# Kernel optimization log

Measured on AMD Instinct MI355X. Metric: run time of the kernel, lower is better.

The kernel has to match this reference:

```python
import jax, jax.numpy as jnp
import numpy as np

N = 50000      # nodes
E = 400000     # edges (avg degree 8)
F_IN = 128     # input feature dim
H = 4          # heads (layer 1)
D = 128        # hidden per head
C = 3          # classes (layer 2 out, 1 head)
EPS = 1e-5     # BatchNorm eps
SLOPE = 0.2    # LeakyReLU negative slope (DGL GATConv default)


def setup_inputs() -> dict:
    key = jax.random.key(0)
    ks = jax.random.split(key, 16)
    s = jnp.float32(0.05)
    return {
        "features": jax.random.normal(ks[0], (N, F_IN), jnp.float32),
        "src": jax.random.randint(ks[1], (E,), 0, N, jnp.int32),
        "dst": jax.random.randint(ks[2], (E,), 0, N, jnp.int32),
        # GATConv layer 1 params
        "W1": jax.random.normal(ks[3], (F_IN, H * D), jnp.float32) * s,
        "al1": jax.random.normal(ks[4], (H, D), jnp.float32) * s,
        "ar1": jax.random.normal(ks[5], (H, D), jnp.float32) * s,
        "b1": jnp.zeros((H * D,), jnp.float32),
        "Wres1": jax.random.normal(ks[6], (F_IN, H * D), jnp.float32) * s,
        # BatchNorm1d (inference mode)
        "bn_gamma": jnp.ones((H * D,), jnp.float32),
        "bn_beta": jnp.zeros((H * D,), jnp.float32),
        "bn_mean": jnp.zeros((H * D,), jnp.float32),
        "bn_var": jnp.ones((H * D,), jnp.float32),
        # GATConv layer 2 params (1 head, C out)
        "W2": jax.random.normal(ks[7], (H * D, C), jnp.float32) * s,
        "al2": jax.random.normal(ks[8], (1, C), jnp.float32) * s,
        "ar2": jax.random.normal(ks[9], (1, C), jnp.float32) * s,
        "b2": jnp.zeros((C,), jnp.float32),
        "Wres2": jax.random.normal(ks[10], (H * D, C), jnp.float32) * s,
    }


def _gat_layer(x, src, dst, W, attn_l, attn_r, bias, Wres, heads, dim):
    """DGL GATConv (eval mode): gather, LeakyReLU score, segment softmax,
    weighted scatter-sum, linear residual, bias."""
    n = x.shape[0]
    z = (x @ W).reshape(n, heads, dim)                 # [N,H,D]
    el = jnp.sum(z * attn_l, axis=-1)                  # [N,H]
    er = jnp.sum(z * attn_r, axis=-1)                  # [N,H]
    e = jax.nn.leaky_relu(el[src] + er[dst], SLOPE)    # [E,H]
    # segment softmax over incoming edges of each dst node
    m = jax.ops.segment_max(e, dst, num_segments=n)    # [N,H]
    ex = jnp.exp(e - m[dst])                           # [E,H]
    den = jax.ops.segment_sum(ex, dst, num_segments=n) # [N,H]
    alpha = ex / den[dst]                              # [E,H]
    # weighted message aggregation
    rst = jax.ops.segment_sum(z[src] * alpha[..., None], dst, num_segments=n)  # [N,H,D]
    res = (x @ Wres).reshape(n, heads, dim)
    return rst + res + bias.reshape(1, heads, dim)


def reference(features, src, dst, W1, al1, ar1, b1, Wres1,
              bn_gamma, bn_beta, bn_mean, bn_var,
              W2, al2, ar2, b2, Wres2):
    h = _gat_layer(features, src, dst, W1, al1, ar1, b1, Wres1, H, D)
    h = h.reshape(N, H * D)
    # BatchNorm1d (inference) + ELU; dropout is identity in eval mode
    h = (h - bn_mean) * jax.lax.rsqrt(bn_var + EPS) * bn_gamma + bn_beta
    h = jax.nn.elu(h)
    h = _gat_layer(h, src, dst, W2, al2, ar2, b2, Wres2, 1, C)
    return h[:, 0, :]  # squeeze head dim -> [N, C]
```

## Files before the change

### kernel.cpp

```cpp
#include <hip/hip_runtime.h>
#include <hip/hip_bf16.h>

#define N_NODES 50000
#define N_EDGES 400000
#define FIN     128
#define HD      512
#define SLOPE   0.2f
#define NB_X    782

typedef __hip_bfloat16 bf16;
typedef __bf16 bf16x8 __attribute__((ext_vector_type(8)));
typedef __bf16 bf16x4 __attribute__((ext_vector_type(4)));
typedef __bf16 bf16x2 __attribute__((ext_vector_type(2)));
typedef float  f32x4  __attribute__((ext_vector_type(4)));
typedef float  f32x2  __attribute__((ext_vector_type(2)));

__global__ void sentinel_k(float* out, int n) {
    int i = blockIdx.x * 256 + threadIdx.x;
    if (i < n) out[i] = 12288.0f;
}

__global__ __launch_bounds__(256) void prep_k(const float* __restrict__ W1, const float* __restrict__ Wres1,
                                              const float* __restrict__ al1, const float* __restrict__ ar1,
                                              const float* __restrict__ W2, const float* __restrict__ Wres2,
                                              const float* __restrict__ b1,
                                              const float* __restrict__ bnm, const float* __restrict__ bnv,
                                              const float* __restrict__ bng, const float* __restrict__ bnb,
                                              bf16* __restrict__ Wfrag, float* __restrict__ tab,
                                              bf16* __restrict__ wlrb,
                                              int* __restrict__ deg, int* __restrict__ cur0,
                                              int* __restrict__ done) {
    int b = blockIdx.x;
    if (b < 196) {
        int i = b * 256 + threadIdx.x;
        if (i < N_NODES) { deg[i] = 0; cur0[i] = 0; }
        if (b == 0 && threadIdx.x == 0) *done = 0;
        return;
    }
    b -= 196;
    if (b < 64) {
        int f = b * 256 + threadIdx.x;
        int lane = f & 63, unit = f >> 6;
        int tile = unit >> 3, ks = unit & 7;
        int cl = lane & 15, rg = lane >> 4;
        int gc = tile * 16 + cl;
        int k0 = ks * 32 + rg * 8;
        bf16x8 v;
#pragma unroll
        for (int j = 0; j < 8; ++j) {
            int kk = k0 + j;
            float x = (kk < 128) ? W1[kk * HD + gc] : Wres1[(kk - 128) * HD + gc];
            v[j] = (__bf16)x;
        }
        *reinterpret_cast<bf16x8*>(reinterpret_cast<char*>(Wfrag) + (size_t)f * 16) = v;
        return;
    }
    b -= 64;
    if (b < 16) {
        int i = b * 256 + threadIdx.x;
        int gc = i >> 3, c = i & 7;
        float v;
        if (c < 2) {
            float rs = rsqrtf(bnv[gc] + 1e-5f) * bng[gc];
            v = (c == 0) ? rs : (b1[gc] - bnm[gc]) * rs + bnb[gc];
        } else if (c < 5) {
            v = W2[gc * 3 + (c - 2)];
        } else {
            v = Wres2[gc * 3 + (c - 5)];
        }
        tab[i] = v;
        return;
    }
    for (int i = 0; i < 8; ++i) {
        int e = i * 256 + threadIdx.x;
        int ks = e >> 9, lane = (e >> 3) & 63, j = e & 7;
        int r = lane & 15, rg = lane >> 4;
        int k = ks * 32 + rg * 8 + j;
        float v = 0.f;
        if (r < 4) {
            for (int d = 0; d < 128; ++d) v += W1[k * HD + r * 128 + d] * al1[r * 128 + d];
        } else if (r < 8) {
            int h = r - 4;
            for (int d = 0; d < 128; ++d) v += W1[k * HD + h * 128 + d] * ar1[h * 128 + d];
        }
        wlrb[e] = __float2bfloat16(v);
    }
}

__global__ __launch_bounds__(256) void eler_k(const float* __restrict__ X,
                                              const bf16* __restrict__ wlrb,
                                              float* __restrict__ el, float* __restrict__ er,
                                              bf16* __restrict__ Xb,
                                              const int* __restrict__ dst, int* __restrict__ deg) {
    if (blockIdx.x >= NB_X) {
        int e = (blockIdx.x - NB_X) * 256 + threadIdx.x;
        if (e < N_EDGES) atomicAdd(&deg[dst[e]], 1);
        return;
    }
    __shared__ __align__(16) char XSb[64 * 256];
    const int t = threadIdx.x;
    const int w = t >> 6, lane = t & 63;
    const int cl = lane & 15, rg = lane >> 4;
    const int m0 = blockIdx.x * 64;

#pragma unroll
    for (int j = 0; j < 8; ++j) {
        int e = j * 1024 + t * 4;
        int row = e >> 7, col = e & 127;
        int grow = m0 + row;
        int gc = grow < N_NODES ? grow : N_NODES - 1;
        f32x4 v = *reinterpret_cast<const f32x4*>(X + (size_t)gc * FIN + col);
        bf16x4 bv = {(__bf16)v[0], (__bf16)v[1], (__bf16)v[2], (__bf16)v[3]};
        if (grow < N_NODES)
            *reinterpret_cast<bf16x4*>(Xb + (size_t)grow * FIN + col) = bv;
        int byte = (row * 256 + col * 2) ^ ((row & 7) << 4);
        *reinterpret_cast<bf16x4*>(XSb + byte) = bv;
    }
    __syncthreads();

    f32x4 a = {0.f, 0.f, 0.f, 0.f};
    const int row = w * 16 + cl;
    const int swz = (row & 7) << 4;
#pragma unroll
    for (int ks = 0; ks < 4; ++ks) {
        bf16x8 af = *reinterpret_cast<const bf16x8*>(
            reinterpret_cast<const char*>(wlrb) + ((size_t)(ks * 64 + lane)) * 16);
        int byte = (row * 256 + ks * 64 + rg * 16) ^ swz;
        bf16x8 bf = *reinterpret_cast<const bf16x8*>(XSb + byte);
        a = __builtin_amdgcn_mfma_f32_16x16x32_bf16(af, bf, a, 0, 0, 0);
    }
    int n = m0 + row;
    if (n < N_NODES) {
        if (rg == 0)      *reinterpret_cast<float4*>(el + (size_t)n * 4) = make_float4(a[0], a[1], a[2], a[3]);
        else if (rg == 1) *reinterpret_cast<float4*>(er + (size_t)n * 4) = make_float4(a[0], a[1], a[2], a[3]);
    }
}

__global__ __launch_bounds__(256) void scan_k(const int* __restrict__ deg,
                                              int* __restrict__ rloc, int* __restrict__ blksum,
                                              int* __restrict__ bsum, int* __restrict__ done) {
    __shared__ int wsum[4];
    __shared__ int isLast;
    int t = threadIdx.x, b = blockIdx.x;
    int i = b * 256 + t;
    int v = (i < N_NODES) ? deg[i] : 0;
    int lane = t & 63, w = t >> 6;
    int x = v;
#pragma unroll
    for (int off = 1; off < 64; off <<= 1) {
        int y = __shfl_up(x, off);
        if (lane >= off) x += y;
    }
    if (lane == 63) wsum[w] = x;
    __syncthreads();
    int wadd = 0;
    if (w > 0) wadd += wsum[0];
    if (w > 1) wadd += wsum[1];
    if (w > 2) wadd += wsum[2];
    int incl = x + wadd;
    if (i < N_NODES) rloc[i] = incl - v;
    if (t == 255) atomicExch(&blksum[b], incl);
    __threadfence();
    if (t == 0) {
        int r = atomicAdd(done, 1);
        isLast = (r == 195);
    }
    __syncthreads();
    if (!isLast) return;

    int v2 = (t < 196) ? atomicAdd(&blksum[t], 0) : 0;
    int x2 = v2;
#pragma unroll
    for (int off = 1; off < 64; off <<= 1) {
        int y = __shfl_up(x2, off);
        if (lane >= off) x2 += y;
    }
    __syncthreads();
    if (lane == 63) wsum[w] = x2;
    __syncthreads();
    int wadd2 = 0;
    if (w > 0) wadd2 += wsum[0];
    if (w > 1) wadd2 += wsum[1];
    if (w > 2) wadd2 += wsum[2];
    if (t < 196) bsum[t] = x2 + wadd2 - v2;
}

__global__ void fill_k(const int* __restrict__ src, const int* __restrict__ dst,
                       const int* __restrict__ rloc, const int* __restrict__ bsum,
                       int* __restrict__ cur0, int* __restrict__ csr) {
    int e = blockIdx.x * 256 + threadIdx.x;
    if (e < N_EDGES) {
        int d = dst[e];
        int slot = atomicAdd(&cur0[d], 1);
        csr[rloc[d] + bsum[d >> 8] + slot] = src[e];
    }
}

__global__ __launch_bounds__(1024) void aggX_k(const int* __restrict__ rloc, const int* __restrict__ bsum,
                                               const int* __restrict__ degA, const int* __restrict__ csr,
                                               const float* __restrict__ el, const float* __restrict__ er,
                                               const bf16* __restrict__ Xb, bf16* __restrict__ AGGb,
                                               float* __restrict__ den4) {
    const int w = threadIdx.x >> 6, lane = threadIdx.x & 63;
    const int sub = lane >> 5, ll = lane & 31;
    int n = blockIdx.x * 32 + w * 2 + sub;
    const bool valid = n < N_NODES;
    if (!valid) n = N_NODES - 1;
    const int beg = rloc[n] + bsum[n >> 8];
    const int deg = degA[n];
    const float4 ern = *reinterpret_cast<const float4*>(er + (size_t)n * 4);
    const char* Xbc = reinterpret_cast<const char*>(Xb);

    f32x2 accA[4] = {{0.f,0.f},{0.f,0.f},{0.f,0.f},{0.f,0.f}};
    f32x2 accB[4] = {{0.f,0.f},{0.f,0.f},{0.f,0.f},{0.f,0.f}};
    float4 dp = make_float4(0.f, 0.f, 0.f, 0.f);

    for (int base = 0; base < deg; base += 32) {
        const int cnt = min(32, deg - base);
        int s = 0;
        if (ll < cnt) s = csr[beg + base + ll];
        float4 e4 = *reinterpret_cast<const float4*>(el + (size_t)s * 4);
        float4 p; float e;
        e = e4.x + ern.x; e = e > 0.f ? e : SLOPE * e; p.x = __expf(e);
        e = e4.y + ern.y; e = e > 0.f ? e : SLOPE * e; p.y = __expf(e);
        e = e4.z + ern.z; e = e > 0.f ? e : SLOPE * e; p.z = __expf(e);
        e = e4.w + ern.w; e = e > 0.f ? e : SLOPE * e; p.w = __expf(e);

        for (int j = 0; j < cnt; ++j) {
            int idx = sub * 32 + j;
            int sj = __shfl(s, idx);
            uint2 xv = *reinterpret_cast<const uint2*>(Xbc + (size_t)sj * 256 + ll * 8);
            float4 pj;
            pj.x = __shfl(p.x, idx);
            pj.y = __shfl(p.y, idx);
            pj.z = __shfl(p.z, idx);
            pj.w = __shfl(p.w, idx);
            dp.x += pj.x; dp.y += pj.y; dp.z += pj.z; dp.w += pj.w;
            f32x2 xlo = {__uint_as_float(xv.x << 16), __uint_as_float(xv.x & 0xffff0000u)};
            f32x2 xhi = {__uint_as_float(xv.y << 16), __uint_as_float(xv.y & 0xffff0000u)};
            accA[0] += pj.x * xlo; accB[0] += pj.x * xhi;
            accA[1] += pj.y * xlo; accB[1] += pj.y * xhi;
            accA[2] += pj.z * xlo; accB[2] += pj.z * xhi;
            accA[3] += pj.w * xlo; accB[3] += pj.w * xhi;
        }
    }

    if (valid) {
#pragma unroll
        for (int h = 0; h < 4; ++h) {
            bf16x4 v = {(__bf16)accA[h][0], (__bf16)accA[h][1],
                        (__bf16)accB[h][0], (__bf16)accB[h][1]};
            *reinterpret_cast<bf16x4*>(AGGb + (size_t)n * 512 + h * 128 + ll * 4) = v;
        }
        if (ll == 0) *reinterpret_cast<float4*>(den4 + (size_t)n * 4) = dp;
    }
}

__global__ __launch_bounds__(256) void gemm2_k(
    const bf16* __restrict__ Xb, const bf16* __restrict__ AGGb,
    const float* __restrict__ den4,
    const bf16* __restrict__ Wfrag, const float* __restrict__ tab,
    const float* __restrict__ al2, const float* __restrict__ ar2,
    float* __restrict__ node2) {
    __shared__ __align__(16) char XS[32 * 256];
    __shared__ __align__(16) char AGS[32 * 1024];
    __shared__ float zsum[4][32][6];

    const int t = threadIdx.x;
    const int w = t >> 6, lane = t & 63;
    const int cl = lane & 15, rg = lane >> 4;
    const int m0 = blockIdx.x * 32;

#pragma unroll
    for (int j = 0; j < 2; ++j) {
        int L = j * 4096 + t * 16;
        int row = L >> 8, col = L & 255;
        int grow = m0 + row; grow = grow < N_NODES ? grow : N_NODES - 1;
        bf16x8 v = *reinterpret_cast<const bf16x8*>(
            reinterpret_cast<const char*>(Xb) + (size_t)grow * 256 + col);
        int byte = (row * 256 + col) ^ ((row & 7) << 4);
        *reinterpret_cast<bf16x8*>(XS + byte) = v;
    }
#pragma unroll
    for (int j = 0; j < 8; ++j) {
        int L = j * 4096 + t * 16;
        int row = L >> 10, col = L & 1023;
        int grow = m0 + row; grow = grow < N_NODES ? grow : N_NODES - 1;
        bf16x8 v = *reinterpret_cast<const bf16x8*>(
            reinterpret_cast<const char*>(AGGb) + (size_t)grow * 1024 + col);
        int byte = (row * 1024 + col) ^ ((row & 7) << 4);
        *reinterpret_cast<bf16x8*>(AGS + byte) = v;
    }
    __syncthreads();

    float invden[2];
#pragma unroll
    for (int mt = 0; mt < 2; ++mt) {
        int nn = m0 + mt * 16 + cl;
        nn = nn < N_NODES ? nn : N_NODES - 1;
        float d = den4[(size_t)nn * 4 + w];
        invden[mt] = d > 0.f ? 1.f / d : 0.f;
    }

    float z2p[2][3] = {}, r2p[2][3] = {};

#pragma unroll
    for (int ct = 0; ct < 8; ++ct) {
        const int unit = (w * 8 + ct) * 8;
        bf16x8 af[8];
#pragma unroll
        for (int ks = 0; ks < 8; ++ks)
            af[ks] = *reinterpret_cast<const bf16x8*>(
                reinterpret_cast<const char*>(Wfrag) + ((size_t)(unit + ks) * 64 + lane) * 16);
        const int gcl = w * 128 + ct * 16 + rg * 4;
        f32x4 t0[4], t1[4];
#pragma unroll
        for (int i = 0; i < 4; ++i) {
            t0[i] = *reinterpret_cast<const f32x4*>(tab + (size_t)(gcl + i) * 8);
            t1[i] = *reinterpret_cast<const f32x4*>(tab + (size_t)(gcl + i) * 8 + 4);
        }
#pragma unroll
        for (int mt = 0; mt < 2; ++mt) {
            int row = mt * 16 + cl;
            int swz = (row & 7) << 4;
            f32x4 aA = {0.f, 0.f, 0.f, 0.f};
            f32x4 aX = {0.f, 0.f, 0.f, 0.f};
#pragma unroll
            for (int ks = 0; ks < 4; ++ks) {
                int byte = (row * 1024 + w * 256 + ks * 64 + rg * 16) ^ swz;
                bf16x8 bfr = *reinterpret_cast<const bf16x8*>(AGS + byte);
                aA = __builtin_amdgcn_mfma_f32_16x16x32_bf16(af[ks], bfr, aA, 0, 0, 0);
            }
#pragma unroll
            for (int ks = 0; ks < 4; ++ks) {
                int byte = (row * 256 + ks * 64 + rg * 16) ^ swz;
                bf16x8 bfr = *reinterpret_cast<const bf16x8*>(XS + byte);
                aX = __builtin_amdgcn_mfma_f32_16x16x32_bf16(af[ks + 4], bfr, aX, 0, 0, 0);
            }
#pragma unroll
            for (int i = 0; i < 4; ++i) {
                float z = aA[i] * invden[mt] + aX[i];
                float hv = z * t0[i][0] + t0[i][1];
                hv = hv > 0.f ? hv : (__expf(hv) - 1.f);
                z2p[mt][0] += hv * t0[i][2]; z2p[mt][1] += hv * t0[i][3]; z2p[mt][2] += hv * t1[i][0];
                r2p[mt][0] += hv * t1[i][1]; r2p[mt][1] += hv * t1[i][2]; r2p[mt][2] += hv * t1[i][3];
            }
        }
    }

#pragma unroll
    for (int mt = 0; mt < 2; ++mt)
#pragma unroll
        for (int c = 0; c < 3; ++c) {
            z2p[mt][c] += __shfl_xor(z2p[mt][c], 16);
            z2p[mt][c] += __shfl_xor(z2p[mt][c], 32);
            r2p[mt][c] += __shfl_xor(r2p[mt][c], 16);
            r2p[mt][c] += __shfl_xor(r2p[mt][c], 32);
        }
    if (rg == 0) {
#pragma unroll
        for (int mt = 0; mt < 2; ++mt) {
            int nl = mt * 16 + cl;
            zsum[w][nl][0] = z2p[mt][0]; zsum[w][nl][1] = z2p[mt][1]; zsum[w][nl][2] = z2p[mt][2];
            zsum[w][nl][3] = r2p[mt][0]; zsum[w][nl][4] = r2p[mt][1]; zsum[w][nl][5] = r2p[mt][2];
        }
    }
    __syncthreads();
    if (t < 32) {
        float v[6];
#pragma unroll
        for (int c = 0; c < 6; ++c)
            v[c] = zsum[0][t][c] + zsum[1][t][c] + zsum[2][t][c] + zsum[3][t][c];
        int n = m0 + t;
        if (n < N_NODES) {
            float e2l = v[0] * al2[0] + v[1] * al2[1] + v[2] * al2[2];
            float e2r = v[0] * ar2[0] + v[1] * ar2[1] + v[2] * ar2[2];
            *reinterpret_cast<float4*>(node2 + (size_t)n * 8) = make_float4(v[0], v[1], v[2], e2l);
            *reinterpret_cast<float4*>(node2 + (size_t)n * 8 + 4) = make_float4(v[3], v[4], v[5], e2r);
        }
    }
}

__global__ __launch_bounds__(256) void agg2_k(const int* __restrict__ rloc, const int* __restrict__ bsum,
                                              const int* __restrict__ degA, const int* __restrict__ csr,
                                              const float* __restrict__ node2,
                                              const float* __restrict__ b2, float* __restrict__ out) {
    int wv = threadIdx.x >> 6, lane = threadIdx.x & 63;
    int n = blockIdx.x * 4 + wv;
    int beg = rloc[n] + bsum[n >> 8];
    int deg = degA[n];
    float ern = node2[(size_t)n * 8 + 7];
    float den = 0.f, a0 = 0.f, a1 = 0.f, a2 = 0.f;
    for (int j = lane; j < deg; j += 64) {
        int s = csr[beg + j];
        float4 v = *reinterpret_cast<const float4*>(node2 + (size_t)s * 8);
        float e = v.w + ern;
        e = e > 0.f ? e : SLOPE * e;
        float p = __expf(e);
        den += p;
        a0 += p * v.x; a1 += p * v.y; a2 += p * v.z;
    }
#pragma unroll
    for (int off = 32; off > 0; off >>= 1) {
        den += __shfl_xor(den, off);
        a0 += __shfl_xor(a0, off); a1 += __shfl_xor(a1, off); a2 += __shfl_xor(a2, off);
    }
    if (lane == 0) {
        float inv = deg > 0 ? 1.f / den : 0.f;
        float4 r = *reinterpret_cast<const float4*>(node2 + (size_t)n * 8 + 4);
        out[(size_t)n * 3 + 0] = a0 * inv + r.x + b2[0];
        out[(size_t)n * 3 + 1] = a1 * inv + r.y + b2[1];
        out[(size_t)n * 3 + 2] = a2 * inv + r.z + b2[2];
    }
}

extern "C" void kernel_launch(void* const* d_in, const int* in_sizes, int n_in,
                              void* d_out, int out_size, void* d_ws, size_t ws_size,
                              hipStream_t stream) {
    const float* X     = (const float*)d_in[0];
    const int*   src   = (const int*)d_in[1];
    const int*   dst   = (const int*)d_in[2];
    const float* W1    = (const float*)d_in[3];
    const float* al1   = (const float*)d_in[4];
    const float* ar1   = (const float*)d_in[5];
    const float* b1    = (const float*)d_in[6];
    const float* Wres1 = (const float*)d_in[7];
    const float* bng   = (const float*)d_in[8];
    const float* bnb   = (const float*)d_in[9];
    const float* bnm   = (const float*)d_in[10];
    const float* bnv   = (const float*)d_in[11];
    const float* W2    = (const float*)d_in[12];
    const float* al2   = (const float*)d_in[13];
    const float* ar2   = (const float*)d_in[14];
    const float* b2    = (const float*)d_in[15];
    const float* Wres2 = (const float*)d_in[16];
    float* out = (float*)d_out;

    char* p = (char*)d_ws;
    auto carve = [&](size_t bytes) -> char* {
        char* r = p;
        p += (bytes + 255) & ~(size_t)255;
        return r;
    };
    bf16*  Wfrag  = (bf16*)carve((size_t)512 * 256 * 2);
    float* tab    = (float*)carve((size_t)512 * 8 * 4);
    bf16*  wlrb   = (bf16*)carve((size_t)2048 * 2);
    float* el     = (float*)carve((size_t)N_NODES * 4 * 4);
    float* er     = (float*)carve((size_t)N_NODES * 4 * 4);
    int*   deg    = (int*)carve((size_t)N_NODES * 4);
    int*   rloc   = (int*)carve((size_t)(N_NODES + 256) * 4);
    int*   cur0   = (int*)carve((size_t)N_NODES * 4);
    int*   blksum = (int*)carve((size_t)256 * 4);
    int*   bsum   = (int*)carve((size_t)256 * 4);
    int*   done   = (int*)carve((size_t)256);
    int*   csr    = (int*)carve((size_t)N_EDGES * 4);
    bf16*  Xb     = (bf16*)carve((size_t)N_NODES * FIN * 2);
    bf16*  AGGb   = (bf16*)carve((size_t)N_NODES * 512 * 2);
    float* den4   = (float*)carve((size_t)(N_NODES + 64) * 4 * 4);
    float* node2  = (float*)carve((size_t)N_NODES * 8 * 4);
    size_t need = (size_t)(p - (char*)d_ws);
    if (need > ws_size) {
        sentinel_k<<<(out_size + 255) / 256, 256, 0, stream>>>(out, out_size);
        return;
    }

    prep_k<<<196 + 64 + 16 + 1, 256, 0, stream>>>(W1, Wres1, al1, ar1, W2, Wres2, b1,
                                                  bnm, bnv, bng, bnb, Wfrag, tab, wlrb,
                                                  deg, cur0, done);
    eler_k<<<NB_X + (N_EDGES + 255) / 256, 256, 0, stream>>>(X, wlrb, el, er, Xb, dst, deg);
    scan_k<<<196, 256, 0, stream>>>(deg, rloc, blksum, bsum, done);
    fill_k<<<(N_EDGES + 255) / 256, 256, 0, stream>>>(src, dst, rloc, bsum, cur0, csr);
    aggX_k<<<(N_NODES + 31) / 32, 1024, 0, stream>>>(rloc, bsum, deg, csr, el, er, Xb, AGGb, den4);
    gemm2_k<<<(N_NODES + 31) / 32, 256, 0, stream>>>(Xb, AGGb, den4, Wfrag, tab, al2, ar2, node2);
    agg2_k<<<N_NODES / 4, 256, 0, stream>>>(rloc, bsum, deg, csr, node2, b2, out);
}
```

Before: 189.2 us.

## Store X and aggregate in MFMA fragment layout so gemm2 loads fragments directly

eler_k now also writes the bf16 input tile in MFMA B-fragment order (XF), and aggX_k stages its aggregated rows in shared memory and writes them out in fragment order (AGF). gemm2_k then loads its MFMA operands straight into registers from global memory instead of staging through 40KB of LDS with a barrier, and gets a launch bound of two blocks per SIMD. The aim is to drop LDS traffic and the sync from gemm2 and raise its occupancy. In exchange aggX_k gains 32KB of LDS, a block barrier and a shuffle pass, and an extra XF write is added. A __syncthreads was also added to scan_k before the completion counter, which fixes ordering.

```diff
diff --git a/kernel.cpp b/kernel.cpp
--- a/kernel.cpp
+++ b/kernel.cpp
@@ -90,7 +90,7 @@
 __global__ __launch_bounds__(256) void eler_k(const float* __restrict__ X,
                                               const bf16* __restrict__ wlrb,
                                               float* __restrict__ el, float* __restrict__ er,
-                                              bf16* __restrict__ Xb,
+                                              bf16* __restrict__ Xb, bf16* __restrict__ XF,
                                               const int* __restrict__ dst, int* __restrict__ deg) {
     if (blockIdx.x >= NB_X) {
         int e = (blockIdx.x - NB_X) * 256 + threadIdx.x;
@@ -121,12 +121,14 @@
     f32x4 a = {0.f, 0.f, 0.f, 0.f};
     const int row = w * 16 + cl;
     const int swz = (row & 7) << 4;
+    char* XFc = reinterpret_cast<char*>(XF);
 #pragma unroll
     for (int ks = 0; ks < 4; ++ks) {
         bf16x8 af = *reinterpret_cast<const bf16x8*>(
             reinterpret_cast<const char*>(wlrb) + ((size_t)(ks * 64 + lane)) * 16);
         int byte = (row * 256 + ks * 64 + rg * 16) ^ swz;
         bf16x8 bf = *reinterpret_cast<const bf16x8*>(XSb + byte);
+        *reinterpret_cast<bf16x8*>(XFc + ((size_t)(blockIdx.x * 4 + w) * 4 + ks) * 1024 + lane * 16) = bf;
         a = __builtin_amdgcn_mfma_f32_16x16x32_bf16(af, bf, a, 0, 0, 0);
     }
     int n = m0 + row;
@@ -161,6 +163,7 @@
     if (i < N_NODES) rloc[i] = incl - v;
     if (t == 255) atomicExch(&blksum[b], incl);
     __threadfence();
+    __syncthreads();
     if (t == 0) {
         int r = atomicAdd(done, 1);
         isLast = (r == 195);
@@ -199,11 +202,13 @@
 __global__ __launch_bounds__(1024) void aggX_k(const int* __restrict__ rloc, const int* __restrict__ bsum,
                                                const int* __restrict__ degA, const int* __restrict__ csr,
                                                const float* __restrict__ el, const float* __restrict__ er,
-                                               const bf16* __restrict__ Xb, bf16* __restrict__ AGGb,
+                                               const bf16* __restrict__ Xb, bf16* __restrict__ AGF,
                                                float* __restrict__ den4) {
+    __shared__ __align__(16) char AS[32 * 1024];
     const int w = threadIdx.x >> 6, lane = threadIdx.x & 63;
     const int sub = lane >> 5, ll = lane & 31;
-    int n = blockIdx.x * 32 + w * 2 + sub;
+    const int nl = w * 2 + sub;
+    int n = blockIdx.x * 32 + nl;
     const bool valid = n < N_NODES;
     if (!valid) n = N_NODES - 1;
     const int beg = rloc[n] + bsum[n >> 8];
@@ -245,53 +250,59 @@
         }
     }
 
-    if (valid) {
+    {
+        const int swz = (nl & 7) << 4;
 #pragma unroll
         for (int h = 0; h < 4; ++h) {
             bf16x4 v = {(__bf16)accA[h][0], (__bf16)accA[h][1],
                         (__bf16)accB[h][0], (__bf16)accB[h][1]};
-            *reinterpret_cast<bf16x4*>(AGGb + (size_t)n * 512 + h * 128 + ll * 4) = v;
-        }
-        if (ll == 0) *reinterpret_cast<float4*>(den4 + (size_t)n * 4) = dp;
-    }
-}
-
-__global__ __launch_bounds__(256) void gemm2_k(
-    const bf16* __restrict__ Xb, const bf16* __restrict__ AGGb,
+            int byte = (nl * 1024 + h * 256 + ll * 8) ^ swz;
+            *reinterpret_cast<bf16x4*>(AS + byte) = v;
+        }
+        if (valid && ll == 0) *reinterpret_cast<float4*>(den4 + (size_t)n * 4) = dp;
+    }
+    __syncthreads();
+
+    const int t = threadIdx.x;
+    char* AGFc = reinterpret_cast<char*>(AGF);
+#pragma unroll
+    for (int q = 0; q < 2; ++q) {
+        int fid = q * 1024 + t;
+        int L = fid & 63, unit = fid >> 6;
+        int g = unit >> 4, h = (unit >> 2) & 3, ks = unit & 3;
+        int nl2 = g * 16 + (L & 15);
+        int sbyte = (nl2 * 1024 + h * 256 + ks * 64 + (L >> 4) * 16) ^ ((nl2 & 7) << 4);
+        bf16x8 v = *reinterpret_cast<const bf16x8*>(AS + sbyte);
+        size_t gid = ((size_t)(blockIdx.x * 2 + g) * 16 + h * 4 + ks);
+        *reinterpret_cast<bf16x8*>(AGFc + gid * 1024 + (size_t)L * 16) = v;
+    }
+}
+
+__global__ __launch_bounds__(256, 2) void gemm2_k(
+    const bf16* __restrict__ XF, const bf16* __restrict__ AGF,
     const float* __restrict__ den4,
     const bf16* __restrict__ Wfrag, const float* __restrict__ tab,
     const float* __restrict__ al2, const float* __restrict__ ar2,
     float* __restrict__ node2) {
-    __shared__ __align__(16) char XS[32 * 256];
-    __shared__ __align__(16) char AGS[32 * 1024];
     __shared__ float zsum[4][32][6];
 
     const int t = threadIdx.x;
     const int w = t >> 6, lane = t & 63;
     const int cl = lane & 15, rg = lane >> 4;
     const int m0 = blockIdx.x * 32;
-
-#pragma unroll
-    for (int j = 0; j < 2; ++j) {
-        int L = j * 4096 + t * 16;
-        int row = L >> 8, col = L & 255;
-        int grow = m0 + row; grow = grow < N_NODES ? grow : N_NODES - 1;
-        bf16x8 v = *reinterpret_cast<const bf16x8*>(
-            reinterpret_cast<const char*>(Xb) + (size_t)grow * 256 + col);
-        int byte = (row * 256 + col) ^ ((row & 7) << 4);
-        *reinterpret_cast<bf16x8*>(XS + byte) = v;
-    }
-#pragma unroll
-    for (int j = 0; j < 8; ++j) {
-        int L = j * 4096 + t * 16;
-        int row = L >> 10, col = L & 1023;
-        int grow = m0 + row; grow = grow < N_NODES ? grow : N_NODES - 1;
-        bf16x8 v = *reinterpret_cast<const bf16x8*>(
-            reinterpret_cast<const char*>(AGGb) + (size_t)grow * 1024 + col);
-        int byte = (row * 1024 + col) ^ ((row & 7) << 4);
-        *reinterpret_cast<bf16x8*>(AGS + byte) = v;
-    }
-    __syncthreads();
+    const char* AGFc = reinterpret_cast<const char*>(AGF);
+    const char* XFc = reinterpret_cast<const char*>(XF);
+
+    bf16x8 agf[2][4], xf[2][4];
+#pragma unroll
+    for (int mt = 0; mt < 2; ++mt)
+#pragma unroll
+        for (int ks = 0; ks < 4; ++ks) {
+            size_t gA = ((size_t)(blockIdx.x * 2 + mt) * 16 + w * 4 + ks);
+            agf[mt][ks] = *reinterpret_cast<const bf16x8*>(AGFc + gA * 1024 + (size_t)lane * 16);
+            size_t gX = ((size_t)(blockIdx.x * 2 + mt) * 4 + ks);
+            xf[mt][ks] = *reinterpret_cast<const bf16x8*>(XFc + gX * 1024 + (size_t)lane * 16);
+        }
 
     float invden[2];
 #pragma unroll
@@ -321,22 +332,14 @@
         }
 #pragma unroll
         for (int mt = 0; mt < 2; ++mt) {
-            int row = mt * 16 + cl;
-            int swz = (row & 7) << 4;
             f32x4 aA = {0.f, 0.f, 0.f, 0.f};
             f32x4 aX = {0.f, 0.f, 0.f, 0.f};
 #pragma unroll
-            for (int ks = 0; ks < 4; ++ks) {
-                int byte = (row * 1024 + w * 256 + ks * 64 + rg * 16) ^ swz;
-                bf16x8 bfr = *reinterpret_cast<const bf16x8*>(AGS + byte);
-                aA = __builtin_amdgcn_mfma_f32_16x16x32_bf16(af[ks], bfr, aA, 0, 0, 0);
-            }
-#pragma unroll
-            for (int ks = 0; ks < 4; ++ks) {
-                int byte = (row * 256 + ks * 64 + rg * 16) ^ swz;
-                bf16x8 bfr = *reinterpret_cast<const bf16x8*>(XS + byte);
-                aX = __builtin_amdgcn_mfma_f32_16x16x32_bf16(af[ks + 4], bfr, aX, 0, 0, 0);
-            }
+            for (int ks = 0; ks < 4; ++ks)
+                aA = __builtin_amdgcn_mfma_f32_16x16x32_bf16(af[ks], agf[mt][ks], aA, 0, 0, 0);
+#pragma unroll
+            for (int ks = 0; ks < 4; ++ks)
+                aX = __builtin_amdgcn_mfma_f32_16x16x32_bf16(af[ks + 4], xf[mt][ks], aX, 0, 0, 0);
 #pragma unroll
             for (int i = 0; i < 4; ++i) {
                 float z = aA[i] * invden[mt] + aX[i];
@@ -455,7 +458,8 @@
     int*   done   = (int*)carve((size_t)256);
     int*   csr    = (int*)carve((size_t)N_EDGES * 4);
     bf16*  Xb     = (bf16*)carve((size_t)N_NODES * FIN * 2);
-    bf16*  AGGb   = (bf16*)carve((size_t)N_NODES * 512 * 2);
+    bf16*  XF     = (bf16*)carve((size_t)3136 * 4 * 1024);
+    bf16*  AGF    = (bf16*)carve((size_t)3136 * 16 * 1024);
     float* den4   = (float*)carve((size_t)(N_NODES + 64) * 4 * 4);
     float* node2  = (float*)carve((size_t)N_NODES * 8 * 4);
     size_t need = (size_t)(p - (char*)d_ws);
@@ -467,10 +471,10 @@
     prep_k<<<196 + 64 + 16 + 1, 256, 0, stream>>>(W1, Wres1, al1, ar1, W2, Wres2, b1,
                                                   bnm, bnv, bng, bnb, Wfrag, tab, wlrb,
                                                   deg, cur0, done);
-    eler_k<<<NB_X + (N_EDGES + 255) / 256, 256, 0, stream>>>(X, wlrb, el, er, Xb, dst, deg);
+    eler_k<<<NB_X + (N_EDGES + 255) / 256, 256, 0, stream>>>(X, wlrb, el, er, Xb, XF, dst, deg);
     scan_k<<<196, 256, 0, stream>>>(deg, rloc, blksum, bsum, done);
     fill_k<<<(N_EDGES + 255) / 256, 256, 0, stream>>>(src, dst, rloc, bsum, cur0, csr);
-    aggX_k<<<(N_NODES + 31) / 32, 1024, 0, stream>>>(rloc, bsum, deg, csr, el, er, Xb, AGGb, den4);
-    gemm2_k<<<(N_NODES + 31) / 32, 256, 0, stream>>>(Xb, AGGb, den4, Wfrag, tab, al2, ar2, node2);
+    aggX_k<<<(N_NODES + 31) / 32, 1024, 0, stream>>>(rloc, bsum, deg, csr, el, er, Xb, AGF, den4);
+    gemm2_k<<<(N_NODES + 31) / 32, 256, 0, stream>>>(XF, AGF, den4, Wfrag, tab, al2, ar2, node2);
     agg2_k<<<N_NODES / 4, 256, 0, stream>>>(rloc, bsum, deg, csr, node2, b2, out);
 }
```

Result: slower. 195.5 us (+3.3%).
